# Kernel optimization log

Hardware: AMD Instinct MI355X
Metric: run time of the kernel (lower is better)

## Reference

```python
import jax, jax.numpy as jnp
import numpy as np

# NeuralVolume(num_levels=4, level_dim=8, base_resolution=16, per_level_scale=2)
RESOLUTIONS = [16, 32, 64, 128]          # ceil(16 * 2**l) per level
LEVEL_DIM = 8                             # C
OFFSETS = np.concatenate([[0], np.cumsum([r ** 3 for r in RESOLUTIONS])]).astype(np.int64)
N_PARAMS = int(OFFSETS[-1])               # 2,396,160 (dense grids, no hashing: R^3 << 2^24)
B = 1 << 20
# 8 cube corners, d=0 is the fastest-varying (stride-1) dim as in the CUDA kernel
CORNERS = np.array([[i, j, k] for k in (0, 1) for j in (0, 1) for i in (0, 1)], np.int32)


def setup_inputs() -> dict:
    key = jax.random.key(0)
    k1, k2 = jax.random.split(key)
    inputs = jax.random.uniform(k1, (B, 3), dtype=jnp.float32)          # coords in [0,1)
    embeddings = jax.random.normal(k2, (N_PARAMS, LEVEL_DIM), dtype=jnp.float32) * 1e-4
    return {"inputs": inputs, "embeddings": embeddings}


def _encode_level(x, table, R):
    # x: [B,3] in [0,1]; table: [R^3, C] dense grid for this level
    scale = jnp.float32(R - 1)
    pos = x * scale                                   # [B,3]
    pg = jnp.floor(pos)
    frac = pos - pg                                   # [B,3] trilinear fractions
    pg = pg.astype(jnp.int32)
    corners = jnp.asarray(CORNERS)                    # [8,3]
    cg = jnp.clip(pg[:, None, :] + corners[None], 0, R - 1)   # [B,8,3]
    # linear index with stride 1 along d=0 (index += pos_grid[d]*stride; stride *= R)
    idx = cg[..., 0] + cg[..., 1] * R + cg[..., 2] * (R * R)  # [B,8]
    w = jnp.prod(jnp.where(corners[None] == 1, frac[:, None, :], 1.0 - frac[:, None, :]), axis=-1)  # [B,8]
    feats = table[idx]                                # [B,8,C] irregular gather
    return jnp.einsum('bk,bkc->bc', w, feats)         # [B,C]


def reference(inputs, embeddings):
    outs = []
    for l, R in enumerate(RESOLUTIONS):
        table = jax.lax.dynamic_slice_in_dim(embeddings, int(OFFSETS[l]), int(OFFSETS[l + 1] - OFFSETS[l]), axis=0)
        outs.append(_encode_level(inputs, table, R))
    return jnp.concatenate(outs, axis=-1)             # [B, L*C] = [B, 32]
```

## Files before the change

### kernel.cpp

```cpp
#include <hip/hip_runtime.h>

#define LEVEL_DIM 8
#define CDIM 32
#define NCELLS (CDIM*CDIM*CDIM)
#define NGROUPS (NCELLS/8)

#define SLAB_ROWS 1307

typedef float    f32x4 __attribute__((ext_vector_type(4)));
typedef unsigned u32x4 __attribute__((ext_vector_type(4)));

__device__ __forceinline__ unsigned part1by2(unsigned x) {
    x &= 0x3ff;
    x = (x | (x << 16)) & 0x030000FF;
    x = (x | (x << 8))  & 0x0300F00F;
    x = (x | (x << 4))  & 0x030C30C3;
    x = (x | (x << 2))  & 0x09249249;
    return x;
}
__device__ __forceinline__ unsigned compact1by2(unsigned x) {
    x &= 0x09249249;
    x = (x | (x >> 2))  & 0x030C30C3;
    x = (x | (x >> 4))  & 0x0300F00F;
    x = (x | (x >> 8))  & 0x030000FF;
    x = (x | (x >> 16)) & 0x000003FF;
    return x;
}

__device__ __forceinline__ int cell_of(float x, float y, float z) {
    int cx = min(CDIM - 1, max(0, (int)(x * (float)CDIM)));
    int cy = min(CDIM - 1, max(0, (int)(y * (float)CDIM)));
    int cz = min(CDIM - 1, max(0, (int)(z * (float)CDIM)));
    return (int)(part1by2(cx) | (part1by2(cy) << 1) | (part1by2(cz) << 2));
}

__device__ __forceinline__ unsigned pk_bf16(float a, float b) {
    unsigned ua = __float_as_uint(a), ub = __float_as_uint(b);
    ua += 0x7fffu + ((ua >> 16) & 1u);
    ub += 0x7fffu + ((ub >> 16) & 1u);
    return (ua >> 16) | (ub & 0xffff0000u);
}

__global__ __launch_bounds__(256) void nv_hist(
    const float* __restrict__ in, int* __restrict__ hist,
    unsigned* __restrict__ cellrank, int B)
{
    const int b = blockIdx.x * 256 + threadIdx.x;
    if (b >= B) return;
    const float x = in[3 * b], y = in[3 * b + 1], z = in[3 * b + 2];
    const int c = cell_of(x, y, z);
    const unsigned r = (unsigned)atomicAdd(&hist[c], 1);
    cellrank[b] = (unsigned)c | (r << 15);
}

__global__ __launch_bounds__(1024) void nv_scan(int* __restrict__ cell)
{
    __shared__ int lds[1024];
    const int tid = threadIdx.x;
    const int base = tid * (NCELLS / 1024);
    int v[NCELLS / 1024];
    int s = 0;
    #pragma unroll
    for (int e = 0; e < NCELLS / 1024; ++e) { v[e] = cell[base + e]; s += v[e]; }
    lds[tid] = s;
    __syncthreads();
    for (int off = 1; off < 1024; off <<= 1) {
        int t = 0;
        if (tid >= off) t = lds[tid - off];
        __syncthreads();
        if (tid >= off) lds[tid] += t;
        __syncthreads();
    }
    int run = lds[tid] - s;
    #pragma unroll
    for (int e = 0; e < NCELLS / 1024; ++e) { cell[base + e] = run; run += v[e]; }
}

__global__ __launch_bounds__(256) void nv_scatter(
    const float* __restrict__ in, const int* __restrict__ starts,
    const unsigned* __restrict__ cellrank, f32x4* __restrict__ sorted, int B)
{
    const int b = blockIdx.x * 256 + threadIdx.x;
    if (b >= B) return;
    const float x = in[3 * b], y = in[3 * b + 1], z = in[3 * b + 2];
    const unsigned cr = cellrank[b];
    const int pos = starts[cr & 0x7fffu] + (int)(cr >> 15);
    f32x4 v = { x, y, z, __uint_as_float((unsigned)b) };
    sorted[pos] = v;
}


template<int R, int S, int BASE, int TOFF>
__device__ __forceinline__ void stage_level(
    const float* __restrict__ emb, unsigned* slab,
    int s0x, int s0y, int s0z, int tid)
{
    const float* tbl = emb + (size_t)TOFF * LEVEL_DIM;
    constexpr int ROWS = S * S * S;
    #pragma unroll
    for (int t0 = 0; t0 < ROWS; t0 += 256) {
        const int t = t0 + tid;
        if (t < ROWS) {
            const int lx = t % S;
            const int tm = t / S;
            const int ly = tm % S;
            const int lz = tm / S;
            const float* src = tbl +
                ((size_t)((s0z + lz) * R + (s0y + ly)) * R + (s0x + lx)) * LEVEL_DIM;
            const f32x4 a = *(const f32x4*)src;
            const f32x4 b = *(const f32x4*)(src + 4);
            u32x4 d = { pk_bf16(a.x, a.y), pk_bf16(a.z, a.w),
                        pk_bf16(b.x, b.y), pk_bf16(b.z, b.w) };
            *(u32x4*)&slab[(BASE + t) * 4] = d;
        }
    }
}

__global__ __launch_bounds__(256) void nv_encode_group(
    const f32x4* __restrict__ sorted,
    const int* __restrict__ starts,
    const float* __restrict__ emb,
    float* __restrict__ out,
    int B)
{
    __shared__ __align__(16) unsigned slab[SLAB_ROWS * 4];

    int grp = (int)blockIdx.x;
    grp = (grp & 7) * (NGROUPS / 8) + (grp >> 3);

    const int c0 = grp << 3;
    const int start = starts[c0];
    const int end   = (c0 + 8 < NCELLS) ? starts[c0 + 8] : B;
    if (start >= end) return;

    const int gx = (int)compact1by2((unsigned)grp);
    const int gy = (int)compact1by2((unsigned)grp >> 1);
    const int gz = (int)compact1by2((unsigned)grp >> 2);

    const int s0x0 = min((gx * 30)  >> 5, 13),  s0y0 = min((gy * 30)  >> 5, 13),  s0z0 = min((gz * 30)  >> 5, 13);
    const int s0x1 = min((gx * 62)  >> 5, 28),  s0y1 = min((gy * 62)  >> 5, 28),  s0z1 = min((gz * 62)  >> 5, 28);
    const int s0x2 = min((gx * 126) >> 5, 58),  s0y2 = min((gy * 126) >> 5, 58),  s0z2 = min((gz * 126) >> 5, 58);
    const int s0x3 = min((gx * 254) >> 5, 118), s0y3 = min((gy * 254) >> 5, 118), s0z3 = min((gz * 254) >> 5, 118);

    const int tid = threadIdx.x;
    stage_level<16,  3,  0,   0>     (emb, slab, s0x0, s0y0, s0z0, tid);
    stage_level<32,  4,  27,  4096>  (emb, slab, s0x1, s0y1, s0z1, tid);
    stage_level<64,  6,  91,  36864> (emb, slab, s0x2, s0y2, s0z2, tid);
    stage_level<128, 10, 307, 299008>(emb, slab, s0x3, s0y3, s0z3, tid);
    __syncthreads();

    const int ln  = tid & 7;
    const int lvl = ln >> 1;
    const int sub = tid >> 3;

    #define SEL4(v0,v1,v2,v3) ((lvl & 2) ? ((lvl & 1) ? (v3) : (v2)) \
                                         : ((lvl & 1) ? (v1) : (v0)))
    const float scale = SEL4(15.0f, 31.0f, 63.0f, 127.0f);
    const int   Rm1   = SEL4(15, 31, 63, 127);
    const int   S_    = SEL4(3, 4, 6, 10);
    const int   BASE_ = SEL4(0, 27, 91, 307);
    const int   sx    = SEL4(s0x0, s0x1, s0x2, s0x3);
    const int   sy    = SEL4(s0y0, s0y1, s0y2, s0y3);
    const int   sz    = SEL4(s0z0, s0z1, s0z2, s0z3);
    #undef SEL4
    const int dsel = (ln & 1) * 2;

    for (int p = start + sub; p < end; p += 32) {
        const f32x4 s = sorted[p];
        const unsigned ob = __float_as_uint(s.w);

        const float px = s.x * scale, py = s.y * scale, pz = s.z * scale;
        const float gpx = floorf(px), gpy = floorf(py), gpz = floorf(pz);
        const float fx = px - gpx, fy = py - gpy, fz = pz - gpz;
        const int ix = (int)gpx, iy = (int)gpy, iz = (int)gpz;

        const int ix0 = min(max(ix, 0), Rm1),     ix1 = min(max(ix + 1, 0), Rm1);
        const int iy0 = min(max(iy, 0), Rm1),     iy1 = min(max(iy + 1, 0), Rm1);
        const int iz0 = min(max(iz, 0), Rm1),     iz1 = min(max(iz + 1, 0), Rm1);

        const int lx0 = ix0 - sx, lx1 = ix1 - sx;
        const int ly0 = iy0 - sy, ly1 = iy1 - sy;
        const int lz0 = iz0 - sz, lz1 = iz1 - sz;

        const float wx0 = 1.0f - fx, wx1 = fx;
        const float wy0 = 1.0f - fy, wy1 = fy;
        const float wz0 = 1.0f - fz, wz1 = fz;

        const int rzy00 = BASE_ + (lz0 * S_ + ly0) * S_;
        const int rzy01 = BASE_ + (lz0 * S_ + ly1) * S_;
        const int rzy10 = BASE_ + (lz1 * S_ + ly0) * S_;
        const int rzy11 = BASE_ + (lz1 * S_ + ly1) * S_;

        float a0 = 0.0f, a1 = 0.0f, a2 = 0.0f, a3 = 0.0f;

        #define CORNER(rzy, lx, wx, wy, wz) do {                              \
            const uint2 d = *(const uint2*)&slab[((rzy) + (lx)) * 4 + dsel];  \
            const float w = ((wx) * (wy)) * (wz);                             \
            a0 = fmaf(w, __uint_as_float(d.x << 16),         a0);             \
            a1 = fmaf(w, __uint_as_float(d.x & 0xffff0000u), a1);             \
            a2 = fmaf(w, __uint_as_float(d.y << 16),         a2);             \
            a3 = fmaf(w, __uint_as_float(d.y & 0xffff0000u), a3);             \
        } while (0)

        CORNER(rzy00, lx0, wx0, wy0, wz0);
        CORNER(rzy00, lx1, wx1, wy0, wz0);
        CORNER(rzy01, lx0, wx0, wy1, wz0);
        CORNER(rzy01, lx1, wx1, wy1, wz0);
        CORNER(rzy10, lx0, wx0, wy0, wz1);
        CORNER(rzy10, lx1, wx1, wy0, wz1);
        CORNER(rzy11, lx0, wx0, wy1, wz1);
        CORNER(rzy11, lx1, wx1, wy1, wz1);
        #undef CORNER

        const f32x4 r = { a0, a1, a2, a3 };
        __builtin_nontemporal_store(
            r, (f32x4*)(out + (size_t)ob * 32 + ln * 4));
    }
}

__global__ __launch_bounds__(256) void nv_encode_direct(
    const float* __restrict__ in,
    const float* __restrict__ emb,
    float* __restrict__ out,
    int B)
{
    const int i = blockIdx.x * 256 + threadIdx.x;
    if (i >= B) return;
    const float x = in[3 * i], y = in[3 * i + 1], z = in[3 * i + 2];
    float* op = out + (size_t)i * 32;

    const int RES[4] = {16, 32, 64, 128};
    const int OFF[4] = {0, 4096, 36864, 299008};

    #pragma unroll
    for (int l = 0; l < 4; ++l) {
        const int R = RES[l];
        const float scale = (float)(R - 1);
        const float px = x * scale, py = y * scale, pz = z * scale;
        const float gxf = floorf(px), gyf = floorf(py), gzf = floorf(pz);
        const float fx = px - gxf, fy = py - gyf, fz = pz - gzf;
        const int ix = (int)gxf, iy = (int)gyf, iz = (int)gzf;
        const int ix0 = min(max(ix, 0), R - 1), ix1 = min(max(ix + 1, 0), R - 1);
        const int iy0 = min(max(iy, 0), R - 1), iy1 = min(max(iy + 1, 0), R - 1);
        const int iz0 = min(max(iz, 0), R - 1), iz1 = min(max(iz + 1, 0), R - 1);
        const float* tbl = emb + (size_t)OFF[l] * LEVEL_DIM;
        const float wx0 = 1.0f - fx, wx1 = fx;
        float acc[8];
        #pragma unroll
        for (int c = 0; c < 8; ++c) acc[c] = 0.0f;
        #pragma unroll
        for (int kk = 0; kk < 2; ++kk) {
            const int zz = kk ? iz1 : iz0;
            const float wz = kk ? fz : (1.0f - fz);
            #pragma unroll
            for (int jj = 0; jj < 2; ++jj) {
                const int yy = jj ? iy1 : iy0;
                const float wy = jj ? fy : (1.0f - fy);
                const size_t rowbase = ((size_t)zz * R + yy) * (size_t)R;
                const float* r0 = tbl + (rowbase + ix0) * LEVEL_DIM;
                const float* r1 = tbl + (rowbase + ix1) * LEVEL_DIM;
                const float w0 = (wx0 * wy) * wz;
                const float w1 = (wx1 * wy) * wz;
                const float4 a0 = *(const float4*)(r0);
                const float4 a1 = *(const float4*)(r0 + 4);
                const float4 b0 = *(const float4*)(r1);
                const float4 b1 = *(const float4*)(r1 + 4);
                acc[0] = fmaf(w0, a0.x, acc[0]); acc[1] = fmaf(w0, a0.y, acc[1]);
                acc[2] = fmaf(w0, a0.z, acc[2]); acc[3] = fmaf(w0, a0.w, acc[3]);
                acc[4] = fmaf(w0, a1.x, acc[4]); acc[5] = fmaf(w0, a1.y, acc[5]);
                acc[6] = fmaf(w0, a1.z, acc[6]); acc[7] = fmaf(w0, a1.w, acc[7]);
                acc[0] = fmaf(w1, b0.x, acc[0]); acc[1] = fmaf(w1, b0.y, acc[1]);
                acc[2] = fmaf(w1, b0.z, acc[2]); acc[3] = fmaf(w1, b0.w, acc[3]);
                acc[4] = fmaf(w1, b1.x, acc[4]); acc[5] = fmaf(w1, b1.y, acc[5]);
                acc[6] = fmaf(w1, b1.z, acc[6]); acc[7] = fmaf(w1, b1.w, acc[7]);
            }
        }
        *(float4*)(op + l * 8)     = make_float4(acc[0], acc[1], acc[2], acc[3]);
        *(float4*)(op + l * 8 + 4) = make_float4(acc[4], acc[5], acc[6], acc[7]);
    }
}

extern "C" void kernel_launch(void* const* d_in, const int* in_sizes, int n_in,
                              void* d_out, int out_size, void* d_ws, size_t ws_size,
                              hipStream_t stream) {
    const float* in  = (const float*)d_in[0];
    const float* emb = (const float*)d_in[1];
    float* out = (float*)d_out;

    const int B = in_sizes[0] / 3;
    const int block = 256;
    const int grid = (B + block - 1) / block;

    const size_t hist_bytes = (size_t)NCELLS * sizeof(int);
    const size_t rank_bytes = (size_t)B * sizeof(unsigned);
    const size_t need = hist_bytes + rank_bytes + (size_t)B * sizeof(f32x4);

    if (ws_size >= need) {
        int*      hist     = (int*)d_ws;
        unsigned* cellrank = (unsigned*)((char*)d_ws + hist_bytes);
        f32x4*    sorted   = (f32x4*)((char*)d_ws + hist_bytes + rank_bytes);

        (void)hipMemsetAsync(hist, 0, hist_bytes, stream);
        nv_hist<<<grid, block, 0, stream>>>(in, hist, cellrank, B);
        nv_scan<<<1, 1024, 0, stream>>>(hist);
        nv_scatter<<<grid, block, 0, stream>>>(in, hist, cellrank, sorted, B);
        nv_encode_group<<<NGROUPS, 256, 0, stream>>>(sorted, hist, emb, out, B);
    } else {
        nv_encode_direct<<<grid, block, 0, stream>>>(in, emb, out, B);
    }
}
```

Before: 122.0 us.

## Replace counting sort with fixed-capacity per-cell buckets plus overflow fixup

```diff
diff --git a/kernel.cpp b/kernel.cpp
--- a/kernel.cpp
+++ b/kernel.cpp
@@ -4,8 +4,15 @@
 #define CDIM 32
 #define NCELLS (CDIM*CDIM*CDIM)
 #define NGROUPS (NCELLS/8)
-
 #define SLAB_ROWS 1307
+
+#define OVF_CAP      65536
+#define COUNTS_BYTES (NCELLS * 4)
+#define OVFCNT_OFF   COUNTS_BYTES
+#define OVF_OFF      (COUNTS_BYTES + 256)
+#define BUCKETS_OFF  (OVF_OFF + OVF_CAP * 16)
+#define CAP_MIN      36
+#define CAP_MAX      64
 
 typedef float    f32x4 __attribute__((ext_vector_type(4)));
 typedef unsigned u32x4 __attribute__((ext_vector_type(4)));
@@ -41,54 +48,24 @@
     return (ua >> 16) | (ub & 0xffff0000u);
 }
 
-__global__ __launch_bounds__(256) void nv_hist(
-    const float* __restrict__ in, int* __restrict__ hist,
-    unsigned* __restrict__ cellrank, int B)
+__global__ __launch_bounds__(256) void nv_bucket(
+    const float* __restrict__ in, int* __restrict__ counts,
+    int* __restrict__ ovf_cnt, f32x4* __restrict__ ovf,
+    f32x4* __restrict__ buckets, int CAP, int B)
 {
     const int b = blockIdx.x * 256 + threadIdx.x;
     if (b >= B) return;
     const float x = in[3 * b], y = in[3 * b + 1], z = in[3 * b + 2];
     const int c = cell_of(x, y, z);
-    const unsigned r = (unsigned)atomicAdd(&hist[c], 1);
-    cellrank[b] = (unsigned)c | (r << 15);
-}
-
-__global__ __launch_bounds__(1024) void nv_scan(int* __restrict__ cell)
-{
-    __shared__ int lds[1024];
-    const int tid = threadIdx.x;
-    const int base = tid * (NCELLS / 1024);
-    int v[NCELLS / 1024];
-    int s = 0;
-    #pragma unroll
-    for (int e = 0; e < NCELLS / 1024; ++e) { v[e] = cell[base + e]; s += v[e]; }
-    lds[tid] = s;
-    __syncthreads();
-    for (int off = 1; off < 1024; off <<= 1) {
-        int t = 0;
-        if (tid >= off) t = lds[tid - off];
-        __syncthreads();
-        if (tid >= off) lds[tid] += t;
-        __syncthreads();
-    }
-    int run = lds[tid] - s;
-    #pragma unroll
-    for (int e = 0; e < NCELLS / 1024; ++e) { cell[base + e] = run; run += v[e]; }
-}
-
-__global__ __launch_bounds__(256) void nv_scatter(
-    const float* __restrict__ in, const int* __restrict__ starts,
-    const unsigned* __restrict__ cellrank, f32x4* __restrict__ sorted, int B)
-{
-    const int b = blockIdx.x * 256 + threadIdx.x;
-    if (b >= B) return;
-    const float x = in[3 * b], y = in[3 * b + 1], z = in[3 * b + 2];
-    const unsigned cr = cellrank[b];
-    const int pos = starts[cr & 0x7fffu] + (int)(cr >> 15);
+    const int r = atomicAdd(&counts[c], 1);
     f32x4 v = { x, y, z, __uint_as_float((unsigned)b) };
-    sorted[pos] = v;
-}
-
+    if (r < CAP) {
+        buckets[(size_t)c * CAP + r] = v;
+    } else {
+        const int o = atomicAdd(ovf_cnt, 1);
+        if (o < OVF_CAP) ovf[o] = v;
+    }
+}
 
 template<int R, int S, int BASE, int TOFF>
 __device__ __forceinline__ void stage_level(
@@ -116,22 +93,31 @@
     }
 }
 
-__global__ __launch_bounds__(256) void nv_encode_group(
-    const f32x4* __restrict__ sorted,
-    const int* __restrict__ starts,
+__global__ __launch_bounds__(256) void nv_encode_bucket(
+    const f32x4* __restrict__ buckets,
+    const int* __restrict__ counts,
     const float* __restrict__ emb,
     float* __restrict__ out,
-    int B)
+    int CAP, int B)
 {
     __shared__ __align__(16) unsigned slab[SLAB_ROWS * 4];
 
     int grp = (int)blockIdx.x;
     grp = (grp & 7) * (NGROUPS / 8) + (grp >> 3);
-
     const int c0 = grp << 3;
-    const int start = starts[c0];
-    const int end   = (c0 + 8 < NCELLS) ? starts[c0 + 8] : B;
-    if (start >= end) return;
+
+    const int cw0 = min(counts[c0 + 0], CAP);
+    const int cw1 = min(counts[c0 + 1], CAP);
+    const int cw2 = min(counts[c0 + 2], CAP);
+    const int cw3 = min(counts[c0 + 3], CAP);
+    const int cw4 = min(counts[c0 + 4], CAP);
+    const int cw5 = min(counts[c0 + 5], CAP);
+    const int cw6 = min(counts[c0 + 6], CAP);
+    const int cw7 = min(counts[c0 + 7], CAP);
+    const int pf1 = cw0,       pf2 = pf1 + cw1, pf3 = pf2 + cw2, pf4 = pf3 + cw3;
+    const int pf5 = pf4 + cw4, pf6 = pf5 + cw5, pf7 = pf6 + cw6;
+    const int total = pf7 + cw7;
+    if (total == 0) return;
 
     const int gx = (int)compact1by2((unsigned)grp);
     const int gy = (int)compact1by2((unsigned)grp >> 1);
@@ -165,8 +151,18 @@
     #undef SEL4
     const int dsel = (ln & 1) * 2;
 
-    for (int p = start + sub; p < end; p += 32) {
-        const f32x4 s = sorted[p];
+    for (int q = sub; q < total; q += 32) {
+        int k = 0, pfk = 0;
+        if (q >= pf1) { k = 1; pfk = pf1; }
+        if (q >= pf2) { k = 2; pfk = pf2; }
+        if (q >= pf3) { k = 3; pfk = pf3; }
+        if (q >= pf4) { k = 4; pfk = pf4; }
+        if (q >= pf5) { k = 5; pfk = pf5; }
+        if (q >= pf6) { k = 6; pfk = pf6; }
+        if (q >= pf7) { k = 7; pfk = pf7; }
+        const int idx = q - pfk;
+
+        const f32x4 s = buckets[(size_t)(c0 + k) * CAP + idx];
         const unsigned ob = __float_as_uint(s.w);
 
         const float px = s.x * scale, py = s.y * scale, pz = s.z * scale;
@@ -218,17 +214,9 @@
     }
 }
 
-__global__ __launch_bounds__(256) void nv_encode_direct(
-    const float* __restrict__ in,
-    const float* __restrict__ emb,
-    float* __restrict__ out,
-    int B)
-{
-    const int i = blockIdx.x * 256 + threadIdx.x;
-    if (i >= B) return;
-    const float x = in[3 * i], y = in[3 * i + 1], z = in[3 * i + 2];
-    float* op = out + (size_t)i * 32;
-
+__device__ __forceinline__ void encode_point_direct(
+    float x, float y, float z, const float* __restrict__ emb, float* op)
+{
     const int RES[4] = {16, 32, 64, 128};
     const int OFF[4] = {0, 4096, 36864, 299008};
 
@@ -280,6 +268,30 @@
     }
 }
 
+__global__ __launch_bounds__(256) void nv_fixup(
+    const int* __restrict__ ovf_cnt, const f32x4* __restrict__ ovf,
+    const float* __restrict__ emb, float* __restrict__ out)
+{
+    const int n = min(*ovf_cnt, OVF_CAP);
+    for (int i = blockIdx.x * 256 + threadIdx.x; i < n; i += gridDim.x * 256) {
+        const f32x4 s = ovf[i];
+        encode_point_direct(s.x, s.y, s.z, emb,
+                            out + (size_t)__float_as_uint(s.w) * 32);
+    }
+}
+
+__global__ __launch_bounds__(256) void nv_encode_direct(
+    const float* __restrict__ in,
+    const float* __restrict__ emb,
+    float* __restrict__ out,
+    int B)
+{
+    const int i = blockIdx.x * 256 + threadIdx.x;
+    if (i >= B) return;
+    encode_point_direct(in[3 * i], in[3 * i + 1], in[3 * i + 2],
+                        emb, out + (size_t)i * 32);
+}
+
 extern "C" void kernel_launch(void* const* d_in, const int* in_sizes, int n_in,
                               void* d_out, int out_size, void* d_ws, size_t ws_size,
                               hipStream_t stream) {
@@ -291,20 +303,21 @@
     const int block = 256;
     const int grid = (B + block - 1) / block;
 
-    const size_t hist_bytes = (size_t)NCELLS * sizeof(int);
-    const size_t rank_bytes = (size_t)B * sizeof(unsigned);
-    const size_t need = hist_bytes + rank_bytes + (size_t)B * sizeof(f32x4);
+    const size_t need = (size_t)BUCKETS_OFF + (size_t)CAP_MIN * NCELLS * 16;
 
     if (ws_size >= need) {
-        int*      hist     = (int*)d_ws;
-        unsigned* cellrank = (unsigned*)((char*)d_ws + hist_bytes);
-        f32x4*    sorted   = (f32x4*)((char*)d_ws + hist_bytes + rank_bytes);
-
-        (void)hipMemsetAsync(hist, 0, hist_bytes, stream);
-        nv_hist<<<grid, block, 0, stream>>>(in, hist, cellrank, B);
-        nv_scan<<<1, 1024, 0, stream>>>(hist);
-        nv_scatter<<<grid, block, 0, stream>>>(in, hist, cellrank, sorted, B);
-        nv_encode_group<<<NGROUPS, 256, 0, stream>>>(sorted, hist, emb, out, B);
+        int CAP = (int)((ws_size - BUCKETS_OFF) / ((size_t)NCELLS * 16));
+        if (CAP > CAP_MAX) CAP = CAP_MAX;
+
+        int*   counts  = (int*)d_ws;
+        int*   ovf_cnt = (int*)((char*)d_ws + OVFCNT_OFF);
+        f32x4* ovf     = (f32x4*)((char*)d_ws + OVF_OFF);
+        f32x4* buckets = (f32x4*)((char*)d_ws + BUCKETS_OFF);
+
+        (void)hipMemsetAsync(d_ws, 0, OVF_OFF, stream);
+        nv_bucket<<<grid, block, 0, stream>>>(in, counts, ovf_cnt, ovf, buckets, CAP, B);
+        nv_encode_bucket<<<NGROUPS, block, 0, stream>>>(buckets, counts, emb, out, CAP, B);
+        nv_fixup<<<128, block, 0, stream>>>(ovf_cnt, ovf, emb, out);
     } else {
         nv_encode_direct<<<grid, block, 0, stream>>>(in, emb, out, B);
     }
```

After: 130.2 us. 6.7% more time.
